# Kernel optimization log

Measured on AMD Instinct MI355X. Metric: run time of the kernel, lower is better.

Reference implementation:

```python
import jax, jax.numpy as jnp
import numpy as np

BS = 128  # block size for weight scale blocks

def dequant_block(w, s):
    # w: [O, I] fp8-valued weights (stored fp32 here); s: [O/BS, I/BS] per-block scale_inv
    O, I = w.shape
    sf = jnp.repeat(jnp.repeat(s, BS, axis=0), BS, axis=1)[:O, :I]
    return w * sf

def setup_inputs() -> dict:
    key = jax.random.key(0)
    ks = jax.random.split(key, 7)
    T, H, F = 512, 7168, 2048
    x = jax.random.normal(ks[0], (T, H), dtype=jnp.float32)
    w_gate = jax.random.normal(ks[1], (F, H), dtype=jnp.float32)
    s_gate = jax.random.uniform(ks[2], (F // BS, H // BS), dtype=jnp.float32, minval=0.01, maxval=0.05)
    w_up = jax.random.normal(ks[3], (F, H), dtype=jnp.float32)
    s_up = jax.random.uniform(ks[4], (F // BS, H // BS), dtype=jnp.float32, minval=0.01, maxval=0.05)
    w_down = jax.random.normal(ks[5], (H, F), dtype=jnp.float32)
    s_down = jax.random.uniform(ks[6], (H // BS, F // BS), dtype=jnp.float32, minval=0.01, maxval=0.05)
    return {"x": x, "w_gate": w_gate, "s_gate": s_gate, "w_up": w_up, "s_up": s_up,
            "w_down": w_down, "s_down": s_down}

def reference(x, w_gate, s_gate, w_up, s_up, w_down, s_down):
    # SwiGLU MLP with block-dequantized FP8 weights: down(silu(gate(x)) * up(x))
    wg = dequant_block(w_gate, s_gate)   # [F, H]
    wu = dequant_block(w_up, s_up)       # [F, H]
    wd = dequant_block(w_down, s_down)   # [H, F]
    g = x @ wg.T                          # [T, F]
    u = x @ wu.T                          # [T, F]
    h = jax.nn.silu(g) * u                # [T, F]
    return h @ wd.T                       # [T, H]
```

## Files before the change

### kernel.cpp

```cpp
#include <hip/hip_runtime.h>
#include <hip/hip_bf16.h>

typedef __bf16 bf16x8_t __attribute__((ext_vector_type(8)));
typedef float f32x4_t __attribute__((ext_vector_type(4)));

#define MFMA_BF16(a, b, c) __builtin_amdgcn_mfma_f32_16x16x32_bf16((a), (b), (c), 0, 0, 0)

static constexpr int T_DIM = 512;
static constexpr int H_DIM = 7168;
static constexpr int F_DIM = 2048;

__device__ __forceinline__ ushort f2bf(float f) {
    return __builtin_bit_cast(ushort, __float2bfloat16(f));
}

__device__ __forceinline__ void gload_lds16(const void* g, void* l) {
    __builtin_amdgcn_global_load_lds(
        (const __attribute__((address_space(1))) unsigned int*)g,
        (__attribute__((address_space(3))) unsigned int*)(uintptr_t)l,
        16, 0, 0);
}

__global__ void cvt_x_kernel(const float* __restrict__ in, ushort* __restrict__ outp, int n4) {
    int i = blockIdx.x * 256 + threadIdx.x;
    if (i < n4) {
        float4 v = reinterpret_cast<const float4*>(in)[i];
        ushort4 o;
        o.x = f2bf(v.x); o.y = f2bf(v.y); o.z = f2bf(v.z); o.w = f2bf(v.w);
        reinterpret_cast<ushort4*>(outp)[i] = o;
    }
}

__global__ __launch_bounds__(256) void gate_up_kernel(
    const ushort* __restrict__ xb, const float* __restrict__ wg,
    const float* __restrict__ sg, const float* __restrict__ wu,
    const float* __restrict__ su, float* __restrict__ gp, int NTS)
{
    __shared__ ushort As[128 * 64];
    __shared__ float  Bs[128 * 64];

    const int tid = threadIdx.x;
    const int lane = tid & 63;
    const int wid = tid >> 6;
    const int wr = wid >> 1, wc = wid & 1;
    const int bn = blockIdx.x, bm = blockIdx.y, bz = blockIdx.z;
    const int m0 = bm * 128;
    const int ks0 = bz * NTS, ks1 = ks0 + NTS;

    const float* __restrict__ Wb = (bn < 16) ? wg : wu;
    const float* __restrict__ srow = ((bn < 16) ? sg : su) + (size_t)(bn & 15) * (H_DIM / 128);
    const int nb = (bn & 15) * 128;

    f32x4_t acc[4][4] = {};

    const int a_row_lo = tid >> 3, a_cu = tid & 7;
    const int b_row_lo = tid >> 4, b_c32 = (tid & 15) >> 1, b_half = tid & 1;

    auto STAGE = [&](int kt) {
        const int k0 = kt * 64;
        #pragma unroll
        for (int q = 0; q < 4; ++q) {
            const int row = q * 32 + a_row_lo;
            gload_lds16(&xb[(size_t)(m0 + row) * H_DIM + k0 + ((a_cu ^ (row & 7)) << 3)],
                        &As[(q * 4096 + tid * 16) >> 1]);
        }
        #pragma unroll
        for (int q = 0; q < 8; ++q) {
            const int row = q * 16 + b_row_lo;
            gload_lds16(&Wb[(size_t)(nb + row) * H_DIM + k0 + ((b_c32 ^ (row & 7)) << 3) + (b_half << 2)],
                        &Bs[(q * 4096 + tid * 16) >> 2]);
        }
    };

    auto COMPUTE = [&](int kt) {
        const float s = srow[kt >> 1];
        #pragma unroll
        for (int ks = 0; ks < 2; ++ks) {
            const int kk = ks * 4 + (lane >> 4);
            bf16x8_t af[4];
            #pragma unroll
            for (int i = 0; i < 4; ++i) {
                const int row = wr * 64 + i * 16 + (lane & 15);
                af[i] = *reinterpret_cast<const bf16x8_t*>(&As[row * 64 + ((kk ^ (row & 7)) << 3)]);
            }
            #pragma unroll
            for (int j = 0; j < 4; ++j) {
                const int row = wc * 64 + j * 16 + (lane & 15);
                const int u32 = kk ^ (row & 7);
                f32x4_t b0 = *reinterpret_cast<const f32x4_t*>(&Bs[row * 64 + u32 * 8]);
                f32x4_t b1 = *reinterpret_cast<const f32x4_t*>(&Bs[row * 64 + u32 * 8 + 4]);
                bf16x8_t bf;
                #pragma unroll
                for (int e = 0; e < 4; ++e) {
                    bf[e]     = (__bf16)(b0[e] * s);
                    bf[e + 4] = (__bf16)(b1[e] * s);
                }
                #pragma unroll
                for (int i = 0; i < 4; ++i)
                    acc[i][j] = MFMA_BF16(af[i], bf, acc[i][j]);
            }
        }
    };

    STAGE(ks0);
    __syncthreads();
    for (int kt = ks0; kt < ks1; ++kt) {
        COMPUTE(kt);
        if (kt + 1 < ks1) {
            __syncthreads();
            STAGE(kt + 1);
            __syncthreads();
        }
    }

    #pragma unroll
    for (int i = 0; i < 4; ++i)
        #pragma unroll
        for (int j = 0; j < 4; ++j)
            #pragma unroll
            for (int r = 0; r < 4; ++r) {
                const int m = m0 + wr * 64 + i * 16 + (lane >> 4) * 4 + r;
                const int nc = bn * 128 + wc * 64 + j * 16 + (lane & 15);
                gp[(size_t)bz * T_DIM * 4096 + (size_t)m * 4096 + nc] = acc[i][j][r];
            }
}

__global__ void h_reduce_kernel(const float* __restrict__ gp, ushort* __restrict__ hb,
                                int nsplit, int n4) {
    int i = blockIdx.x * 256 + threadIdx.x;
    if (i >= n4) return;
    const int m = i >> 9;
    const int c4 = i & 511;
    const size_t base = (size_t)m * 4096 + c4 * 4;
    const size_t stride = (size_t)T_DIM * 4096;
    float4 g = *reinterpret_cast<const float4*>(&gp[base]);
    float4 u = *reinterpret_cast<const float4*>(&gp[base + 2048]);
    for (int s = 1; s < nsplit; ++s) {
        float4 g2 = *reinterpret_cast<const float4*>(&gp[s * stride + base]);
        float4 u2 = *reinterpret_cast<const float4*>(&gp[s * stride + base + 2048]);
        g.x += g2.x; g.y += g2.y; g.z += g2.z; g.w += g2.w;
        u.x += u2.x; u.y += u2.y; u.z += u2.z; u.w += u2.w;
    }
    ushort4 o;
    o.x = f2bf(g.x / (1.0f + __expf(-g.x)) * u.x);
    o.y = f2bf(g.y / (1.0f + __expf(-g.y)) * u.y);
    o.z = f2bf(g.z / (1.0f + __expf(-g.z)) * u.z);
    o.w = f2bf(g.w / (1.0f + __expf(-g.w)) * u.w);
    reinterpret_cast<ushort4*>(hb)[i] = o;
}

__global__ __launch_bounds__(256) void down_kernel(
    const ushort* __restrict__ hb, const float* __restrict__ wd,
    const float* __restrict__ sd, float* __restrict__ out)
{
    __shared__ ushort As[64 * 64];
    __shared__ float  Bs[128 * 64];

    const int tid = threadIdx.x;
    const int lane = tid & 63;
    const int wid = tid >> 6;
    const int wr = wid >> 1, wc = wid & 1;
    const int bn = blockIdx.x, bm = blockIdx.y;
    const int m0 = bm * 64;
    const float* __restrict__ srow = sd + (size_t)bn * (F_DIM / 128);
    const int nb = bn * 128;
    const int NT = F_DIM / 64;

    f32x4_t acc[2][4] = {};

    const int a_row_lo = tid >> 3, a_cu = tid & 7;
    const int b_row_lo = tid >> 4, b_c32 = (tid & 15) >> 1, b_half = tid & 1;

    auto STAGE = [&](int kt) {
        const int k0 = kt * 64;
        #pragma unroll
        for (int q = 0; q < 2; ++q) {
            const int row = q * 32 + a_row_lo;
            gload_lds16(&hb[(size_t)(m0 + row) * F_DIM + k0 + ((a_cu ^ (row & 7)) << 3)],
                        &As[(q * 4096 + tid * 16) >> 1]);
        }
        #pragma unroll
        for (int q = 0; q < 8; ++q) {
            const int row = q * 16 + b_row_lo;
            gload_lds16(&wd[(size_t)(nb + row) * F_DIM + k0 + ((b_c32 ^ (row & 7)) << 3) + (b_half << 2)],
                        &Bs[(q * 4096 + tid * 16) >> 2]);
        }
    };

    auto COMPUTE = [&](int kt) {
        const float s = srow[kt >> 1];
        #pragma unroll
        for (int ks = 0; ks < 2; ++ks) {
            const int kk = ks * 4 + (lane >> 4);
            bf16x8_t af[2];
            #pragma unroll
            for (int i = 0; i < 2; ++i) {
                const int row = wr * 32 + i * 16 + (lane & 15);
                af[i] = *reinterpret_cast<const bf16x8_t*>(&As[row * 64 + ((kk ^ (row & 7)) << 3)]);
            }
            #pragma unroll
            for (int j = 0; j < 4; ++j) {
                const int row = wc * 64 + j * 16 + (lane & 15);
                const int u32 = kk ^ (row & 7);
                f32x4_t b0 = *reinterpret_cast<const f32x4_t*>(&Bs[row * 64 + u32 * 8]);
                f32x4_t b1 = *reinterpret_cast<const f32x4_t*>(&Bs[row * 64 + u32 * 8 + 4]);
                bf16x8_t bf;
                #pragma unroll
                for (int e = 0; e < 4; ++e) {
                    bf[e]     = (__bf16)(b0[e] * s);
                    bf[e + 4] = (__bf16)(b1[e] * s);
                }
                #pragma unroll
                for (int i = 0; i < 2; ++i)
                    acc[i][j] = MFMA_BF16(af[i], bf, acc[i][j]);
            }
        }
    };

    STAGE(0);
    __syncthreads();
    for (int kt = 0; kt < NT; ++kt) {
        COMPUTE(kt);
        if (kt + 1 < NT) {
            __syncthreads();
            STAGE(kt + 1);
            __syncthreads();
        }
    }

    #pragma unroll
    for (int i = 0; i < 2; ++i)
        #pragma unroll
        for (int j = 0; j < 4; ++j)
            #pragma unroll
            for (int r = 0; r < 4; ++r) {
                const int m = m0 + wr * 32 + i * 16 + (lane >> 4) * 4 + r;
                const int nc = nb + wc * 64 + j * 16 + (lane & 15);
                out[(size_t)m * H_DIM + nc] = acc[i][j][r];
            }
}

extern "C" void kernel_launch(void* const* d_in, const int* in_sizes, int n_in,
                              void* d_out, int out_size, void* d_ws, size_t ws_size,
                              hipStream_t stream) {
    const float* x  = (const float*)d_in[0];
    const float* wg = (const float*)d_in[1];
    const float* sg = (const float*)d_in[2];
    const float* wu = (const float*)d_in[3];
    const float* su = (const float*)d_in[4];
    const float* wd = (const float*)d_in[5];
    const float* sd = (const float*)d_in[6];
    float* out = (float*)d_out;

    ushort* xb = (ushort*)d_ws;
    ushort* hb = xb + (size_t)T_DIM * H_DIM;
    float*  gp = (float*)(hb + (size_t)T_DIM * F_DIM);

    const size_t base_b = (size_t)T_DIM * H_DIM * 2 + (size_t)T_DIM * F_DIM * 2;
    const size_t split_b = (size_t)T_DIM * 4096 * 4;

    int nsplit = 1;
    if (ws_size >= base_b + 4 * split_b) nsplit = 4;
    else if (ws_size >= base_b + 2 * split_b) nsplit = 2;

    const int n4x = T_DIM * H_DIM / 4;
    cvt_x_kernel<<<n4x / 256, 256, 0, stream>>>(x, xb, n4x);

    gate_up_kernel<<<dim3(32, T_DIM / 128, nsplit), 256, 0, stream>>>(
        xb, wg, sg, wu, su, gp, (H_DIM / 64) / nsplit);

    const int n4h = T_DIM * F_DIM / 4;
    h_reduce_kernel<<<n4h / 256, 256, 0, stream>>>(gp, hb, nsplit, n4h);

    down_kernel<<<dim3(H_DIM / 128, T_DIM / 64), 256, 0, stream>>>(hb, wd, sd, out);
}
```

Before: 123.8 us.

## Dequantize weights to bf16 at staging time, split-K down GEMM

Weight tiles are now loaded into registers, scaled and converted to bf16 once per tile, and stored in LDS as bf16. This replaces the async fp32 global-to-LDS copy followed by per-warp conversion, halving the B tile's LDS footprint and removing conversion work that each warp repeated. Launch bounds request 4 blocks per CU. The gate/up split-K can grow to 8 when workspace allows, and the down GEMM gains an optional 2-way split-K plus a reduce kernel. The trade-off is that weight loads become synchronous register loads, so they no longer overlap with compute through the async LDS path.

```diff
diff --git a/kernel.cpp b/kernel.cpp
--- a/kernel.cpp
+++ b/kernel.cpp
@@ -31,13 +31,13 @@
     }
 }
 
-__global__ __launch_bounds__(256) void gate_up_kernel(
+__global__ __launch_bounds__(256, 4) void gate_up_kernel(
     const ushort* __restrict__ xb, const float* __restrict__ wg,
     const float* __restrict__ sg, const float* __restrict__ wu,
     const float* __restrict__ su, float* __restrict__ gp, int NTS)
 {
     __shared__ ushort As[128 * 64];
-    __shared__ float  Bs[128 * 64];
+    __shared__ ushort Bs[128 * 64];
 
     const int tid = threadIdx.x;
     const int lane = tid & 63;
@@ -54,7 +54,7 @@
     f32x4_t acc[4][4] = {};
 
     const int a_row_lo = tid >> 3, a_cu = tid & 7;
-    const int b_row_lo = tid >> 4, b_c32 = (tid & 15) >> 1, b_half = tid & 1;
+    const int b_row = tid >> 1, b_half = tid & 1;
 
     auto STAGE = [&](int kt) {
         const int k0 = kt * 64;
@@ -64,20 +64,31 @@
             gload_lds16(&xb[(size_t)(m0 + row) * H_DIM + k0 + ((a_cu ^ (row & 7)) << 3)],
                         &As[(q * 4096 + tid * 16) >> 1]);
         }
-        #pragma unroll
-        for (int q = 0; q < 8; ++q) {
-            const int row = q * 16 + b_row_lo;
-            gload_lds16(&Wb[(size_t)(nb + row) * H_DIM + k0 + ((b_c32 ^ (row & 7)) << 3) + (b_half << 2)],
-                        &Bs[(q * 4096 + tid * 16) >> 2]);
+        const float s = srow[kt >> 1];
+        f32x4_t rb[8];
+        const float* src = &Wb[(size_t)(nb + b_row) * H_DIM + k0 + b_half * 32];
+        #pragma unroll
+        for (int q = 0; q < 8; ++q)
+            rb[q] = reinterpret_cast<const f32x4_t*>(src)[q];
+        #pragma unroll
+        for (int q = 0; q < 4; ++q) {
+            bf16x8_t v;
+            #pragma unroll
+            for (int e = 0; e < 4; ++e) {
+                v[e]     = (__bf16)(rb[2 * q][e] * s);
+                v[e + 4] = (__bf16)(rb[2 * q + 1][e] * s);
+            }
+            const int c16 = b_half * 4 + q;
+            *reinterpret_cast<bf16x8_t*>(
+                &Bs[b_row * 64 + ((c16 ^ (b_row & 7)) << 3)]) = v;
         }
     };
 
-    auto COMPUTE = [&](int kt) {
-        const float s = srow[kt >> 1];
+    auto COMPUTE = [&]() {
         #pragma unroll
         for (int ks = 0; ks < 2; ++ks) {
             const int kk = ks * 4 + (lane >> 4);
-            bf16x8_t af[4];
+            bf16x8_t af[4], bf[4];
             #pragma unroll
             for (int i = 0; i < 4; ++i) {
                 const int row = wr * 64 + i * 16 + (lane & 15);
@@ -86,26 +97,20 @@
             #pragma unroll
             for (int j = 0; j < 4; ++j) {
                 const int row = wc * 64 + j * 16 + (lane & 15);
-                const int u32 = kk ^ (row & 7);
-                f32x4_t b0 = *reinterpret_cast<const f32x4_t*>(&Bs[row * 64 + u32 * 8]);
-                f32x4_t b1 = *reinterpret_cast<const f32x4_t*>(&Bs[row * 64 + u32 * 8 + 4]);
-                bf16x8_t bf;
+                bf[j] = *reinterpret_cast<const bf16x8_t*>(&Bs[row * 64 + ((kk ^ (row & 7)) << 3)]);
+            }
+            #pragma unroll
+            for (int i = 0; i < 4; ++i)
                 #pragma unroll
-                for (int e = 0; e < 4; ++e) {
-                    bf[e]     = (__bf16)(b0[e] * s);
-                    bf[e + 4] = (__bf16)(b1[e] * s);
-                }
-                #pragma unroll
-                for (int i = 0; i < 4; ++i)
-                    acc[i][j] = MFMA_BF16(af[i], bf, acc[i][j]);
-            }
+                for (int j = 0; j < 4; ++j)
+                    acc[i][j] = MFMA_BF16(af[i], bf[j], acc[i][j]);
         }
     };
 
     STAGE(ks0);
     __syncthreads();
     for (int kt = ks0; kt < ks1; ++kt) {
-        COMPUTE(kt);
+        COMPUTE();
         if (kt + 1 < ks1) {
             __syncthreads();
             STAGE(kt + 1);
@@ -149,27 +154,28 @@
     reinterpret_cast<ushort4*>(hb)[i] = o;
 }
 
-__global__ __launch_bounds__(256) void down_kernel(
+template <bool DIRECT>
+__global__ __launch_bounds__(256, 4) void down_kernel(
     const ushort* __restrict__ hb, const float* __restrict__ wd,
-    const float* __restrict__ sd, float* __restrict__ out)
+    const float* __restrict__ sd, float* __restrict__ outp, int NTS)
 {
     __shared__ ushort As[64 * 64];
-    __shared__ float  Bs[128 * 64];
+    __shared__ ushort Bs[128 * 64];
 
     const int tid = threadIdx.x;
     const int lane = tid & 63;
     const int wid = tid >> 6;
     const int wr = wid >> 1, wc = wid & 1;
-    const int bn = blockIdx.x, bm = blockIdx.y;
+    const int bn = blockIdx.x, bm = blockIdx.y, bz = blockIdx.z;
     const int m0 = bm * 64;
     const float* __restrict__ srow = sd + (size_t)bn * (F_DIM / 128);
     const int nb = bn * 128;
-    const int NT = F_DIM / 64;
+    const int ks0 = bz * NTS, ks1 = ks0 + NTS;
 
     f32x4_t acc[2][4] = {};
 
     const int a_row_lo = tid >> 3, a_cu = tid & 7;
-    const int b_row_lo = tid >> 4, b_c32 = (tid & 15) >> 1, b_half = tid & 1;
+    const int b_row = tid >> 1, b_half = tid & 1;
 
     auto STAGE = [&](int kt) {
         const int k0 = kt * 64;
@@ -179,20 +185,31 @@
             gload_lds16(&hb[(size_t)(m0 + row) * F_DIM + k0 + ((a_cu ^ (row & 7)) << 3)],
                         &As[(q * 4096 + tid * 16) >> 1]);
         }
-        #pragma unroll
-        for (int q = 0; q < 8; ++q) {
-            const int row = q * 16 + b_row_lo;
-            gload_lds16(&wd[(size_t)(nb + row) * F_DIM + k0 + ((b_c32 ^ (row & 7)) << 3) + (b_half << 2)],
-                        &Bs[(q * 4096 + tid * 16) >> 2]);
+        const float s = srow[kt >> 1];
+        f32x4_t rb[8];
+        const float* src = &wd[(size_t)(nb + b_row) * F_DIM + k0 + b_half * 32];
+        #pragma unroll
+        for (int q = 0; q < 8; ++q)
+            rb[q] = reinterpret_cast<const f32x4_t*>(src)[q];
+        #pragma unroll
+        for (int q = 0; q < 4; ++q) {
+            bf16x8_t v;
+            #pragma unroll
+            for (int e = 0; e < 4; ++e) {
+                v[e]     = (__bf16)(rb[2 * q][e] * s);
+                v[e + 4] = (__bf16)(rb[2 * q + 1][e] * s);
+            }
+            const int c16 = b_half * 4 + q;
+            *reinterpret_cast<bf16x8_t*>(
+                &Bs[b_row * 64 + ((c16 ^ (b_row & 7)) << 3)]) = v;
         }
     };
 
-    auto COMPUTE = [&](int kt) {
-        const float s = srow[kt >> 1];
+    auto COMPUTE = [&]() {
         #pragma unroll
         for (int ks = 0; ks < 2; ++ks) {
             const int kk = ks * 4 + (lane >> 4);
-            bf16x8_t af[2];
+            bf16x8_t af[2], bf[4];
             #pragma unroll
             for (int i = 0; i < 2; ++i) {
                 const int row = wr * 32 + i * 16 + (lane & 15);
@@ -201,27 +218,21 @@
             #pragma unroll
             for (int j = 0; j < 4; ++j) {
                 const int row = wc * 64 + j * 16 + (lane & 15);
-                const int u32 = kk ^ (row & 7);
-                f32x4_t b0 = *reinterpret_cast<const f32x4_t*>(&Bs[row * 64 + u32 * 8]);
-                f32x4_t b1 = *reinterpret_cast<const f32x4_t*>(&Bs[row * 64 + u32 * 8 + 4]);
-                bf16x8_t bf;
+                bf[j] = *reinterpret_cast<const bf16x8_t*>(&Bs[row * 64 + ((kk ^ (row & 7)) << 3)]);
+            }
+            #pragma unroll
+            for (int i = 0; i < 2; ++i)
                 #pragma unroll
-                for (int e = 0; e < 4; ++e) {
-                    bf[e]     = (__bf16)(b0[e] * s);
-                    bf[e + 4] = (__bf16)(b1[e] * s);
-                }
-                #pragma unroll
-                for (int i = 0; i < 2; ++i)
-                    acc[i][j] = MFMA_BF16(af[i], bf, acc[i][j]);
-            }
+                for (int j = 0; j < 4; ++j)
+                    acc[i][j] = MFMA_BF16(af[i], bf[j], acc[i][j]);
         }
     };
 
-    STAGE(0);
+    STAGE(ks0);
     __syncthreads();
-    for (int kt = 0; kt < NT; ++kt) {
-        COMPUTE(kt);
-        if (kt + 1 < NT) {
+    for (int kt = ks0; kt < ks1; ++kt) {
+        COMPUTE();
+        if (kt + 1 < ks1) {
             __syncthreads();
             STAGE(kt + 1);
             __syncthreads();
@@ -236,8 +247,21 @@
             for (int r = 0; r < 4; ++r) {
                 const int m = m0 + wr * 32 + i * 16 + (lane >> 4) * 4 + r;
                 const int nc = nb + wc * 64 + j * 16 + (lane & 15);
-                out[(size_t)m * H_DIM + nc] = acc[i][j][r];
-            }
+                if (DIRECT)
+                    outp[(size_t)m * H_DIM + nc] = acc[i][j][r];
+                else
+                    outp[(size_t)bz * T_DIM * H_DIM + (size_t)m * H_DIM + nc] = acc[i][j][r];
+            }
+}
+
+__global__ void d_reduce_kernel(const float* __restrict__ dp, float* __restrict__ out, int n4) {
+    int i = blockIdx.x * 256 + threadIdx.x;
+    if (i >= n4) return;
+    const size_t stride4 = (size_t)T_DIM * H_DIM / 4;
+    float4 a = reinterpret_cast<const float4*>(dp)[i];
+    float4 b = reinterpret_cast<const float4*>(dp)[i + stride4];
+    a.x += b.x; a.y += b.y; a.z += b.z; a.w += b.w;
+    reinterpret_cast<float4*>(out)[i] = a;
 }
 
 extern "C" void kernel_launch(void* const* d_in, const int* in_sizes, int n_in,
@@ -260,7 +284,8 @@
     const size_t split_b = (size_t)T_DIM * 4096 * 4;
 
     int nsplit = 1;
-    if (ws_size >= base_b + 4 * split_b) nsplit = 4;
+    if (ws_size >= base_b + 8 * split_b) nsplit = 8;
+    else if (ws_size >= base_b + 4 * split_b) nsplit = 4;
     else if (ws_size >= base_b + 2 * split_b) nsplit = 2;
 
     const int n4x = T_DIM * H_DIM / 4;
@@ -272,5 +297,15 @@
     const int n4h = T_DIM * F_DIM / 4;
     h_reduce_kernel<<<n4h / 256, 256, 0, stream>>>(gp, hb, nsplit, n4h);
 
-    down_kernel<<<dim3(H_DIM / 128, T_DIM / 64), 256, 0, stream>>>(hb, wd, sd, out);
-}
+    const bool dsplit = (size_t)nsplit * split_b >= (size_t)2 * T_DIM * H_DIM * 4;
+    if (dsplit) {
+        float* dp = gp;
+        down_kernel<false><<<dim3(H_DIM / 128, T_DIM / 64, 2), 256, 0, stream>>>(
+            hb, wd, sd, dp, (F_DIM / 64) / 2);
+        const int n4d = T_DIM * H_DIM / 4;
+        d_reduce_kernel<<<n4d / 256, 256, 0, stream>>>(dp, out, n4d);
+    } else {
+        down_kernel<true><<<dim3(H_DIM / 128, T_DIM / 64, 1), 256, 0, stream>>>(
+            hb, wd, sd, out, F_DIM / 64);
+    }
+}
```

Result: slower. 194.0 us (+56.7%).
